# Optimization experiments

Measured on AMD Instinct MI355X. Metric: run time of the kernel, lower is better.

The kernel has to match this reference:

```python
import jax, jax.numpy as jnp
import numpy as np

DELTA_V = 0.5
DELTA_D = 3.0
ALPHA = 1.0
BETA = 1.0
GAMMA = 0.001
K = 5  # max instance label (labels 1..K; 0 = background)


def setup_inputs() -> dict:
    key = jax.random.key(0)
    k1, k2 = jax.random.split(key)
    B, D, H, W = 8, 8, 512, 1024
    embedding = jax.random.normal(k1, (B, D, H, W), dtype=jnp.float32)
    instance_mask = jax.random.randint(k2, (B, H, W), 0, K + 1, dtype=jnp.int32)
    return {"embedding": embedding, "instance_mask": instance_mask}


def _disc_loss(embedding, instance_mask):
    B, D, H, W = embedding.shape
    P = H * W
    emb = embedding.transpose(0, 2, 3, 1).reshape(B, P, D)      # [B,P,D]
    labels = instance_mask.reshape(B, P)                         # [B,P]

    # one-hot over instance labels 1..K (background excluded)
    onehot = (labels[..., None] == jnp.arange(1, K + 1, dtype=labels.dtype)).astype(emb.dtype)  # [B,P,K]
    counts = onehot.sum(axis=1)                                  # [B,K]
    present = counts > 0                                         # [B,K]
    presentf = present.astype(emb.dtype)
    N = presentf.sum(axis=-1)                                    # [B] num instances

    # per-instance centers via segment mean
    sums = jnp.einsum('bpd,bpk->bkd', emb, onehot)               # [B,K,D]
    centers = sums / jnp.maximum(counts, 1.0)[..., None]         # [B,K,D]

    # ---- variance loss: per-pixel distance to own center ----
    idx = jnp.clip(labels - 1, 0, K - 1)                         # [B,P]
    c_pix = jnp.take_along_axis(centers, idx[..., None], axis=1) # [B,P,D]
    d = jnp.sqrt(jnp.sum((emb - c_pix) ** 2, axis=-1))           # [B,P]
    val = jnp.maximum(d - DELTA_V, 0.0) ** 2                     # [B,P]
    inst_sum = jnp.einsum('bp,bpk->bk', val, onehot)             # [B,K]
    inst_mean = inst_sum / jnp.maximum(counts, 1.0)
    loss_var_b = (inst_mean * presentf).sum(-1) / jnp.maximum(N, 1.0)  # [B]

    # ---- distance loss: pairwise center hinge ----
    diff = centers[:, :, None, :] - centers[:, None, :, :]       # [B,K,K,D]
    dist_sq = jnp.sum(diff ** 2, axis=-1)                        # [B,K,K]
    iu = jnp.triu(jnp.ones((K, K), dtype=bool), k=1)             # i<j
    pair_mask = present[:, :, None] & present[:, None, :] & iu   # [B,K,K]
    safe_dist = jnp.sqrt(jnp.where(pair_mask, dist_sq, 1.0))
    term = jnp.maximum(2.0 * DELTA_D - safe_dist, 0.0) ** 2 * pair_mask.astype(emb.dtype)
    n_pairs = N * (N - 1.0) / 2.0
    loss_dist_b = term.sum((-1, -2)) / jnp.where(N > 1, n_pairs, 1.0)  # [B]

    # ---- regularization: mean norm of present centers ----
    c_norm = jnp.sqrt(jnp.where(present, jnp.sum(centers ** 2, axis=-1), 1.0))
    loss_reg_b = (c_norm * presentf).sum(-1) / jnp.maximum(N, 1.0)     # [B]

    # ---- batch mean over images that have at least one instance ----
    has = (N > 0).astype(emb.dtype)                              # [B]
    denom = jnp.maximum(has.sum(), 1.0)
    loss_var = (loss_var_b * has).sum() / denom
    loss_dist = (loss_dist_b * has).sum() / denom
    loss_reg = (loss_reg_b * has).sum() / denom
    total = ALPHA * loss_var + BETA * loss_dist + GAMMA * loss_reg
    return (total, loss_var, loss_dist, loss_reg)


def reference(embedding, instance_mask):
    return _disc_loss(embedding, instance_mask)
```

## Files before the change

### kernel.cpp

```cpp
#include <hip/hip_runtime.h>
#include <math.h>

constexpr int NB   = 8;
constexpr int ND   = 8;
constexpr int NH   = 512;
constexpr int NW   = 1024;
constexpr int NP   = NH * NW;
constexpr int NG   = NP / 4;
constexpr int NK   = 5;

constexpr int BPB1 = 256;
constexpr int GPB1 = NG / BPB1;
constexpr int IT1  = GPB1 / 32;
constexpr int BPB2 = 256;
constexpr int GPB2 = NG / BPB2;

constexpr float DELTA_V     = 0.5f;
constexpr float TWO_DELTA_D = 6.0f;
constexpr float GAMMA       = 0.001f;

__device__ __forceinline__ float wave_sum(float v) {
#pragma unroll
    for (int off = 32; off > 0; off >>= 1) v += __shfl_down(v, off, 64);
    return v;
}

__global__ __launch_bounds__(256) void pass1_kernel(const float* __restrict__ emb,
                                                    const int* __restrict__ mask,
                                                    float* __restrict__ sums,
                                                    float* __restrict__ cnts) {
    const int b    = blockIdx.x / BPB1;
    const int blk  = blockIdx.x % BPB1;
    const int wave = threadIdx.x >> 6;
    const int lane = threadIdx.x & 63;
    const int gl   = lane & 31;
    const int d    = wave * 2 + (lane >> 5);
    const bool dzero = (d == 0);

    const float4* __restrict__ ep = (const float4*)emb + (long)(b * ND + d) * NG;
    const int4*   __restrict__ mp = (const int4*)mask + (long)b * NG;

    float a0 = 0.f, a1 = 0.f, a2 = 0.f, a3 = 0.f, a4 = 0.f;
    float n0 = 0.f, n1 = 0.f, n2 = 0.f, n3 = 0.f, n4 = 0.f;

    const int base = blk * GPB1 + gl;

#define PIX1(LAB, EJ) { const int lab = (LAB); const float ej = (EJ); \
        a0 += (lab == 1) ? ej : 0.f; a1 += (lab == 2) ? ej : 0.f; \
        a2 += (lab == 3) ? ej : 0.f; a3 += (lab == 4) ? ej : 0.f; \
        a4 += (lab == 5) ? ej : 0.f; \
        if (dzero) { n0 += (lab == 1) ? 1.f : 0.f; n1 += (lab == 2) ? 1.f : 0.f; \
                     n2 += (lab == 3) ? 1.f : 0.f; n3 += (lab == 4) ? 1.f : 0.f; \
                     n4 += (lab == 5) ? 1.f : 0.f; } }

#pragma unroll
    for (int it = 0; it < IT1; it += 2) {
        const int ga = base + it * 32;
        const int gb = ga + 32;
        const int4   ma = mp[ga];
        const float4 ea = ep[ga];
        const int4   mb = mp[gb];
        const float4 eb = ep[gb];
        PIX1(ma.x, ea.x) PIX1(ma.y, ea.y) PIX1(ma.z, ea.z) PIX1(ma.w, ea.w)
        PIX1(mb.x, eb.x) PIX1(mb.y, eb.y) PIX1(mb.z, eb.z) PIX1(mb.w, eb.w)
    }
#undef PIX1

#pragma unroll
    for (int off = 16; off > 0; off >>= 1) {
        a0 += __shfl_down(a0, off, 32); a1 += __shfl_down(a1, off, 32);
        a2 += __shfl_down(a2, off, 32); a3 += __shfl_down(a3, off, 32);
        a4 += __shfl_down(a4, off, 32);
    }
    if (wave == 0) {
#pragma unroll
        for (int off = 16; off > 0; off >>= 1) {
            n0 += __shfl_down(n0, off, 32); n1 += __shfl_down(n1, off, 32);
            n2 += __shfl_down(n2, off, 32); n3 += __shfl_down(n3, off, 32);
            n4 += __shfl_down(n4, off, 32);
        }
    }

    __shared__ float pl[ND][NK];
    __shared__ float pc[NK];
    if (gl == 0) {
        pl[d][0] = a0; pl[d][1] = a1; pl[d][2] = a2; pl[d][3] = a3; pl[d][4] = a4;
    }
    if (threadIdx.x == 0) { pc[0] = n0; pc[1] = n1; pc[2] = n2; pc[3] = n3; pc[4] = n4; }
    __syncthreads();
    const int t = threadIdx.x;
    if (t < NK * ND)
        atomicAdd(&sums[b * NK * ND + t], pl[t & 7][t >> 3]);
    else if (t < NK * ND + NK)
        atomicAdd(&cnts[b * NK + (t - NK * ND)], pc[t - NK * ND]);
}

__global__ __launch_bounds__(256) void pass2_kernel(const float* __restrict__ emb,
                                                    const int* __restrict__ mask,
                                                    const float* __restrict__ sums,
                                                    const float* __restrict__ cnts,
                                                    float* __restrict__ vsums) {
    const int b   = blockIdx.x / BPB2;
    const int blk = blockIdx.x % BPB2;
    const long base = (long)blk * GPB2;

    const float* sp = sums + b * NK * ND;
    const float i0 = 1.f / fmaxf(cnts[b * NK + 0], 1.f);
    const float i1 = 1.f / fmaxf(cnts[b * NK + 1], 1.f);
    const float i2 = 1.f / fmaxf(cnts[b * NK + 2], 1.f);
    const float i3 = 1.f / fmaxf(cnts[b * NK + 3], 1.f);
    const float i4 = 1.f / fmaxf(cnts[b * NK + 4], 1.f);
    const float4 c0l = make_float4(sp[0]*i0,  sp[1]*i0,  sp[2]*i0,  sp[3]*i0);
    const float4 c0h = make_float4(sp[4]*i0,  sp[5]*i0,  sp[6]*i0,  sp[7]*i0);
    const float4 c1l = make_float4(sp[8]*i1,  sp[9]*i1,  sp[10]*i1, sp[11]*i1);
    const float4 c1h = make_float4(sp[12]*i1, sp[13]*i1, sp[14]*i1, sp[15]*i1);
    const float4 c2l = make_float4(sp[16]*i2, sp[17]*i2, sp[18]*i2, sp[19]*i2);
    const float4 c2h = make_float4(sp[20]*i2, sp[21]*i2, sp[22]*i2, sp[23]*i2);
    const float4 c3l = make_float4(sp[24]*i3, sp[25]*i3, sp[26]*i3, sp[27]*i3);
    const float4 c3h = make_float4(sp[28]*i3, sp[29]*i3, sp[30]*i3, sp[31]*i3);
    const float4 c4l = make_float4(sp[32]*i4, sp[33]*i4, sp[34]*i4, sp[35]*i4);
    const float4 c4h = make_float4(sp[36]*i4, sp[37]*i4, sp[38]*i4, sp[39]*i4);

    const float4* __restrict__ emb4 = (const float4*)emb + (long)b * ND * NG;
    const int4*   __restrict__ m4p  = (const int4*)mask + (long)b * NG;

    float v0 = 0.f, v1 = 0.f, v2 = 0.f, v3 = 0.f, v4 = 0.f;

    for (int it = threadIdx.x; it < GPB2; it += 256) {
        const long g = base + it;
        const int4   m  = m4p[g];
        const float4 e0 = emb4[g];
        const float4 e1 = emb4[g + (long)NG];
        const float4 e2 = emb4[g + 2L * NG];
        const float4 e3 = emb4[g + 3L * NG];
        const float4 e4 = emb4[g + 4L * NG];
        const float4 e5 = emb4[g + 5L * NG];
        const float4 e6 = emb4[g + 6L * NG];
        const float4 e7 = emb4[g + 7L * NG];

#define SEL2(F) ((lab == 1) ? c0##F : (lab == 2) ? c1##F : (lab == 3) ? c2##F : \
                 (lab == 4) ? c3##F : c4##F)
#define PIX2(LAB, CM) { const int lab = (LAB); \
        float dd = e0.CM - SEL2(l.x); float dsq = dd * dd; \
        dd = e1.CM - SEL2(l.y); dsq = fmaf(dd, dd, dsq); \
        dd = e2.CM - SEL2(l.z); dsq = fmaf(dd, dd, dsq); \
        dd = e3.CM - SEL2(l.w); dsq = fmaf(dd, dd, dsq); \
        dd = e4.CM - SEL2(h.x); dsq = fmaf(dd, dd, dsq); \
        dd = e5.CM - SEL2(h.y); dsq = fmaf(dd, dd, dsq); \
        dd = e6.CM - SEL2(h.z); dsq = fmaf(dd, dd, dsq); \
        dd = e7.CM - SEL2(h.w); dsq = fmaf(dd, dd, dsq); \
        const float dist = sqrtf(dsq); \
        const float hv = fmaxf(dist - DELTA_V, 0.f); \
        const float val = hv * hv; \
        v0 += (lab == 1) ? val : 0.f; v1 += (lab == 2) ? val : 0.f; \
        v2 += (lab == 3) ? val : 0.f; v3 += (lab == 4) ? val : 0.f; \
        v4 += (lab == 5) ? val : 0.f; }

        PIX2(m.x, x) PIX2(m.y, y) PIX2(m.z, z) PIX2(m.w, w)
#undef PIX2
#undef SEL2
    }

    __shared__ float part[4][NK];
    const int lane = threadIdx.x & 63;
    const int wave = threadIdx.x >> 6;
#define RED2(V, IDX) { const float r = wave_sum(V); if (lane == 0) part[wave][IDX] = r; }
    RED2(v0, 0) RED2(v1, 1) RED2(v2, 2) RED2(v3, 3) RED2(v4, 4)
#undef RED2
    __syncthreads();
    if (threadIdx.x < NK) {
        const float s = part[0][threadIdx.x] + part[1][threadIdx.x] +
                        part[2][threadIdx.x] + part[3][threadIdx.x];
        atomicAdd(&vsums[b * NK + threadIdx.x], s);
    }
}

__global__ void final_kernel(const float* __restrict__ sums,
                             const float* __restrict__ cnts,
                             const float* __restrict__ vsums,
                             float* __restrict__ out) {
    __shared__ float bl[4][NB];
    const int bb = threadIdx.x;
    if (bb < NB) {
        float cc[NK];
        bool  pres[NK];
        float c[NK][ND];
        float N = 0.f;
#pragma unroll
        for (int k = 0; k < NK; ++k) {
            cc[k]   = cnts[bb * NK + k];
            pres[k] = cc[k] > 0.f;
            if (pres[k]) N += 1.f;
            const float inv = 1.f / fmaxf(cc[k], 1.f);
#pragma unroll
            for (int d = 0; d < ND; ++d)
                c[k][d] = sums[bb * NK * ND + k * ND + d] * inv;
        }
        float lv = 0.f;
#pragma unroll
        for (int k = 0; k < NK; ++k)
            if (pres[k]) lv += vsums[bb * NK + k] / fmaxf(cc[k], 1.f);
        lv /= fmaxf(N, 1.f);
        float ld = 0.f;
#pragma unroll
        for (int i = 0; i < NK; ++i)
#pragma unroll
            for (int j = i + 1; j < NK; ++j)
                if (pres[i] && pres[j]) {
                    float dsq = 0.f;
#pragma unroll
                    for (int d = 0; d < ND; ++d) {
                        const float df = c[i][d] - c[j][d];
                        dsq = fmaf(df, df, dsq);
                    }
                    const float t = fmaxf(TWO_DELTA_D - sqrtf(dsq), 0.f);
                    ld += t * t;
                }
        const float npairs = N * (N - 1.f) * 0.5f;
        ld /= (N > 1.f) ? npairs : 1.f;
        float lr = 0.f;
#pragma unroll
        for (int k = 0; k < NK; ++k)
            if (pres[k]) {
                float sq = 0.f;
#pragma unroll
                for (int d = 0; d < ND; ++d) sq = fmaf(c[k][d], c[k][d], sq);
                lr += sqrtf(sq);
            }
        lr /= fmaxf(N, 1.f);

        const float has = (N > 0.f) ? 1.f : 0.f;
        bl[0][bb] = lv * has;
        bl[1][bb] = ld * has;
        bl[2][bb] = lr * has;
        bl[3][bb] = has;
    }
    __syncthreads();
    if (threadIdx.x == 0) {
        float tv = 0.f, td = 0.f, tr = 0.f, hs = 0.f;
        for (int i = 0; i < NB; ++i) {
            tv += bl[0][i]; td += bl[1][i]; tr += bl[2][i]; hs += bl[3][i];
        }
        const float denom = fmaxf(hs, 1.f);
        tv /= denom; td /= denom; tr /= denom;
        out[0] = tv + td + GAMMA * tr;
        out[1] = tv;
        out[2] = td;
        out[3] = tr;
    }
}

extern "C" void kernel_launch(void* const* d_in, const int* in_sizes, int n_in,
                              void* d_out, int out_size, void* d_ws, size_t ws_size,
                              hipStream_t stream) {
    const float* emb  = (const float*)d_in[0];
    const int*   mask = (const int*)d_in[1];
    float* out = (float*)d_out;

    float* sums  = (float*)d_ws;
    float* cnts  = sums + NB * NK * ND;
    float* vsums = cnts + NB * NK;

    hipMemsetAsync(d_ws, 0, (size_t)(NB * NK * ND + 2 * NB * NK) * sizeof(float), stream);

    pass1_kernel<<<dim3(NB * BPB1), dim3(256), 0, stream>>>(emb, mask, sums, cnts);
    pass2_kernel<<<dim3(NB * BPB2), dim3(256), 0, stream>>>(emb, mask, sums, cnts, vsums);
    final_kernel<<<1, 64, 0, stream>>>(sums, cnts, vsums, out);
}
```

Measured before the change: 257.4 us.

## Split batch in halves to overlap pass2 of first half with pass1 of second

Splits the batch into two halves and runs three kernels: pass1 on the first half, a mixed kernel doing pass1 on the second half and pass2 on the first half, then pass2 on the second half. The aim is to shrink the dependency barrier between the centroid pass and the variance pass so more work is in flight at each launch boundary. It adds one extra kernel launch and changes the per-block work sizes.

```diff
diff --git a/kernel.cpp b/kernel.cpp
--- a/kernel.cpp
+++ b/kernel.cpp
@@ -8,12 +8,7 @@
 constexpr int NP   = NH * NW;
 constexpr int NG   = NP / 4;
 constexpr int NK   = 5;
-
-constexpr int BPB1 = 256;
-constexpr int GPB1 = NG / BPB1;
-constexpr int IT1  = GPB1 / 32;
-constexpr int BPB2 = 256;
-constexpr int GPB2 = NG / BPB2;
+constexpr int NVAL = NK * ND + NK;
 
 constexpr float DELTA_V     = 0.5f;
 constexpr float TWO_DELTA_D = 6.0f;
@@ -25,12 +20,12 @@
     return v;
 }
 
-__global__ __launch_bounds__(256) void pass1_kernel(const float* __restrict__ emb,
-                                                    const int* __restrict__ mask,
-                                                    float* __restrict__ sums,
-                                                    float* __restrict__ cnts) {
-    const int b    = blockIdx.x / BPB1;
-    const int blk  = blockIdx.x % BPB1;
+template<int GPB>
+__device__ __forceinline__ void p1_body(const float* __restrict__ emb,
+                                        const int* __restrict__ mask,
+                                        float* __restrict__ sums,
+                                        float* __restrict__ cnts,
+                                        const int b, const int blk) {
     const int wave = threadIdx.x >> 6;
     const int lane = threadIdx.x & 63;
     const int gl   = lane & 31;
@@ -43,7 +38,8 @@
     float a0 = 0.f, a1 = 0.f, a2 = 0.f, a3 = 0.f, a4 = 0.f;
     float n0 = 0.f, n1 = 0.f, n2 = 0.f, n3 = 0.f, n4 = 0.f;
 
-    const int base = blk * GPB1 + gl;
+    const int base = blk * GPB + gl;
+    constexpr int IT = GPB / 32;
 
 #define PIX1(LAB, EJ) { const int lab = (LAB); const float ej = (EJ); \
         a0 += (lab == 1) ? ej : 0.f; a1 += (lab == 2) ? ej : 0.f; \
@@ -54,7 +50,7 @@
                      n4 += (lab == 5) ? 1.f : 0.f; } }
 
 #pragma unroll
-    for (int it = 0; it < IT1; it += 2) {
+    for (int it = 0; it < IT; it += 2) {
         const int ga = base + it * 32;
         const int gb = ga + 32;
         const int4   ma = mp[ga];
@@ -91,18 +87,18 @@
     const int t = threadIdx.x;
     if (t < NK * ND)
         atomicAdd(&sums[b * NK * ND + t], pl[t & 7][t >> 3]);
-    else if (t < NK * ND + NK)
+    else if (t < NVAL)
         atomicAdd(&cnts[b * NK + (t - NK * ND)], pc[t - NK * ND]);
 }
 
-__global__ __launch_bounds__(256) void pass2_kernel(const float* __restrict__ emb,
-                                                    const int* __restrict__ mask,
-                                                    const float* __restrict__ sums,
-                                                    const float* __restrict__ cnts,
-                                                    float* __restrict__ vsums) {
-    const int b   = blockIdx.x / BPB2;
-    const int blk = blockIdx.x % BPB2;
-    const long base = (long)blk * GPB2;
+template<int GPB>
+__device__ __forceinline__ void p2_body(const float* __restrict__ emb,
+                                        const int* __restrict__ mask,
+                                        const float* __restrict__ sums,
+                                        const float* __restrict__ cnts,
+                                        float* __restrict__ vsums,
+                                        const int b, const int blk) {
+    const long base = (long)blk * GPB;
 
     const float* sp = sums + b * NK * ND;
     const float i0 = 1.f / fmaxf(cnts[b * NK + 0], 1.f);
@@ -126,7 +122,7 @@
 
     float v0 = 0.f, v1 = 0.f, v2 = 0.f, v3 = 0.f, v4 = 0.f;
 
-    for (int it = threadIdx.x; it < GPB2; it += 256) {
+    for (int it = threadIdx.x; it < GPB; it += 256) {
         const long g = base + it;
         const int4   m  = m4p[g];
         const float4 e0 = emb4[g];
@@ -175,6 +171,42 @@
     }
 }
 
+__global__ __launch_bounds__(256) void p1a_kernel(const float* __restrict__ emb,
+                                                  const int* __restrict__ mask,
+                                                  float* __restrict__ sums,
+                                                  float* __restrict__ cnts) {
+    const int b   = blockIdx.x >> 9;
+    const int blk = blockIdx.x & 511;
+    p1_body<256>(emb, mask, sums, cnts, b, blk);
+}
+
+__global__ __launch_bounds__(256) void mix_kernel(const float* __restrict__ emb,
+                                                  const int* __restrict__ mask,
+                                                  float* __restrict__ sums,
+                                                  float* __restrict__ cnts,
+                                                  float* __restrict__ vsums) {
+    if (blockIdx.x < 1024) {
+        const int b   = 4 + (blockIdx.x >> 8);
+        const int blk = blockIdx.x & 255;
+        p1_body<512>(emb, mask, sums, cnts, b, blk);
+    } else {
+        const int idx = blockIdx.x - 1024;
+        const int b   = idx >> 8;
+        const int blk = idx & 255;
+        p2_body<512>(emb, mask, sums, cnts, vsums, b, blk);
+    }
+}
+
+__global__ __launch_bounds__(256) void p2b_kernel(const float* __restrict__ emb,
+                                                  const int* __restrict__ mask,
+                                                  const float* __restrict__ sums,
+                                                  const float* __restrict__ cnts,
+                                                  float* __restrict__ vsums) {
+    const int b   = 4 + (blockIdx.x >> 9);
+    const int blk = blockIdx.x & 511;
+    p2_body<256>(emb, mask, sums, cnts, vsums, b, blk);
+}
+
 __global__ void final_kernel(const float* __restrict__ sums,
                              const float* __restrict__ cnts,
                              const float* __restrict__ vsums,
@@ -263,7 +295,8 @@
 
     hipMemsetAsync(d_ws, 0, (size_t)(NB * NK * ND + 2 * NB * NK) * sizeof(float), stream);
 
-    pass1_kernel<<<dim3(NB * BPB1), dim3(256), 0, stream>>>(emb, mask, sums, cnts);
-    pass2_kernel<<<dim3(NB * BPB2), dim3(256), 0, stream>>>(emb, mask, sums, cnts, vsums);
+    p1a_kernel<<<dim3(2048), dim3(256), 0, stream>>>(emb, mask, sums, cnts);
+    mix_kernel<<<dim3(2048), dim3(256), 0, stream>>>(emb, mask, sums, cnts, vsums);
+    p2b_kernel<<<dim3(2048), dim3(256), 0, stream>>>(emb, mask, sums, cnts, vsums);
     final_kernel<<<1, 64, 0, stream>>>(sums, cnts, vsums, out);
 }
```

Result: slower. 289.6 us (+12.5%).
